# Performance work log

Hardware: AMD Instinct MI355X
Metric: run time of the kernel (lower is better)

The kernel has to match this reference:

```python
import jax, jax.numpy as jnp
import numpy as np
from jax import lax

D_MODEL = 1024
D_INNER = 2 * D_MODEL          # expand=2
D_STATE = 16
D_CONV = 4
DT_RANK = (D_MODEL + 15) // 16  # ceil(d_model/16) = 64
B, L = 4, 2048
EPS = 1e-6


def setup_inputs() -> dict:
    key = jax.random.key(0)
    ks = jax.random.split(key, 16)
    g = lambda k, shape, s=0.02: jax.random.normal(k, shape, jnp.float32) * s
    A_init = jnp.broadcast_to(jnp.arange(1, D_STATE + 1, dtype=jnp.float32), (D_INNER, D_STATE))
    return {
        "x": jax.random.normal(ks[0], (B, L, D_MODEL), jnp.float32),
        "rms1_w": jnp.ones((D_MODEL,), jnp.float32),
        "rms2_w": jnp.ones((D_MODEL,), jnp.float32),
        "in_proj_w": g(ks[1], (2 * D_INNER, D_MODEL)),
        "conv_w": g(ks[2], (D_INNER, D_CONV), 0.1),
        "conv_b": jnp.zeros((D_INNER,), jnp.float32),
        "x_proj_w": g(ks[3], (DT_RANK + 2 * D_STATE, D_INNER)),
        "dt_proj_w": g(ks[4], (D_INNER, DT_RANK), 0.1),
        "dt_proj_b": jnp.full((D_INNER,), -4.0, jnp.float32),  # softplus -> small dt
        "A_log": jnp.log(A_init),
        "D_skip": jnp.ones((D_INNER,), jnp.float32),
        "out_proj_w": g(ks[5], (D_MODEL, D_INNER)),
        "fc1_w": g(ks[6], (2 * D_MODEL, D_MODEL)),
        "fc1_b": jnp.zeros((2 * D_MODEL,), jnp.float32),
        "fc2_w": g(ks[7], (2 * D_MODEL, 2 * D_MODEL)),
        "fc2_b": jnp.zeros((2 * D_MODEL,), jnp.float32),
        "fc3_w": g(ks[8], (D_MODEL, 2 * D_MODEL)),
        "fc3_b": jnp.zeros((D_MODEL,), jnp.float32),
    }


def _rmsnorm(h, w):
    var = jnp.mean(h.astype(jnp.float32) ** 2, axis=-1, keepdims=True)
    return (w * (h * lax.rsqrt(var + EPS))).astype(h.dtype)


def _mamba(x, in_proj_w, conv_w, conv_b, x_proj_w, dt_proj_w, dt_proj_b, A_log, D_skip, out_proj_w):
    # x: (B, L, D_MODEL)
    xz = jnp.einsum('bld,ed->ble', x, in_proj_w)            # (B, L, 2*D_INNER)
    u, z = jnp.split(xz, 2, axis=-1)                        # each (B, L, D_INNER)
    # causal depthwise conv1d over time
    u_t = jnp.transpose(u, (0, 2, 1))                       # (B, D_INNER, L)
    conv = lax.conv_general_dilated(
        u_t, conv_w[:, None, :], (1,), [(D_CONV - 1, 0)],
        dimension_numbers=('NCH', 'OIH', 'NCH'), feature_group_count=D_INNER)
    u = jax.nn.silu(jnp.transpose(conv + conv_b[None, :, None], (0, 2, 1)))  # (B, L, D_INNER)
    # input-dependent SSM params
    dbc = jnp.einsum('bld,ed->ble', u, x_proj_w)            # (B, L, DT_RANK + 2*D_STATE)
    dt, Bm, Cm = jnp.split(dbc, [DT_RANK, DT_RANK + D_STATE], axis=-1)
    dt = jax.nn.softplus(jnp.einsum('blr,dr->bld', dt, dt_proj_w) + dt_proj_b)  # (B, L, D_INNER)
    A = -jnp.exp(A_log)                                     # (D_INNER, D_STATE)

    def step(s, inp):
        d, u_i, b_i, c_i = inp                              # d,u_i:(B,Di); b_i,c_i:(B,N)
        s = s * jnp.exp(d[..., None] * A) + (d * u_i)[..., None] * b_i[:, None, :]
        y = jnp.einsum('bdn,bn->bd', s, c_i)
        return s, y

    s0 = jnp.zeros((u.shape[0], D_INNER, D_STATE), u.dtype)
    inputs = (jnp.moveaxis(dt, 1, 0), jnp.moveaxis(u, 1, 0),
              jnp.moveaxis(Bm, 1, 0), jnp.moveaxis(Cm, 1, 0))
    _, ys = lax.scan(step, s0, inputs)                      # (L, B, D_INNER)
    y = jnp.moveaxis(ys, 0, 1) + u * D_skip                 # (B, L, D_INNER)
    y = y * jax.nn.silu(z)
    return jnp.einsum('ble,de->bld', y, out_proj_w)         # (B, L, D_MODEL)


def _mlp(x, fc1_w, fc1_b, fc2_w, fc2_b, fc3_w, fc3_b):
    h = jax.nn.relu(jnp.einsum('bld,hd->blh', x, fc1_w) + fc1_b)
    h = jax.nn.relu(jnp.einsum('blh,gh->blg', h, fc2_w) + fc2_b)
    return jnp.einsum('blg,dg->bld', h, fc3_w) + fc3_b


def reference(x, rms1_w, rms2_w, in_proj_w, conv_w, conv_b, x_proj_w, dt_proj_w,
              dt_proj_b, A_log, D_skip, out_proj_w, fc1_w, fc1_b, fc2_w, fc2_b,
              fc3_w, fc3_b):
    x0 = _rmsnorm(x, rms1_w)
    x1 = _mamba(x0, in_proj_w, conv_w, conv_b, x_proj_w, dt_proj_w, dt_proj_b,
                A_log, D_skip, out_proj_w)
    x = x1 + x
    x2 = _rmsnorm(x, rms2_w)
    x3 = _mlp(x2, fc1_w, fc1_b, fc2_w, fc2_b, fc3_w, fc3_b)
    return x + x3
```

## Files before the change

### kernel.cpp

```cpp
#include <hip/hip_runtime.h>
#include <hip/hip_bf16.h>
#include <math.h>

#define D_MODEL 1024
#define D_INNER 2048
#define NSTATE 16
#define DT_RANK 64
#define NB 4
#define SEQ 2048
#define XPROJ_N 96
#define EPSV 1e-6f
#define CH 32
#define CL (SEQ/CH)

typedef __attribute__((ext_vector_type(8))) short bf16x8;
typedef __attribute__((ext_vector_type(4))) float f32x4;

__device__ __forceinline__ float sigmoidf_fast(float x) {
    return 1.f / (1.f + __expf(-x));
}

__device__ __forceinline__ ushort f2bf(float f) {
    union { float f; unsigned int u; } c; c.f = f;
    return (ushort)((c.u + 0x7FFFu + ((c.u >> 16) & 1u)) >> 16);
}

__device__ __forceinline__ float bf2f(ushort u) {
    union { unsigned int i; float f; } c; c.i = ((unsigned int)u) << 16; return c.f;
}

__device__ __forceinline__ float softplus_fast(float v) {
    return fmaxf(v, 0.f) + __logf(1.f + __expf(-fabsf(v)));
}

__device__ __forceinline__ void gload16(const ushort* g, ushort* l) {
    __builtin_amdgcn_global_load_lds(
        (const __attribute__((address_space(1))) unsigned int*)g,
        (__attribute__((address_space(3))) unsigned int*)l, 16, 0, 0);
}

__global__ __launch_bounds__(256)
void cvt_all_kernel(const float* __restrict__ s0, const float* __restrict__ s1,
                    const float* __restrict__ s2, const float* __restrict__ s3,
                    const float* __restrict__ s4, const float* __restrict__ s5,
                    ushort* __restrict__ dst) {
    const size_t i = ((size_t)blockIdx.x * 256 + threadIdx.x) * 4;
    const size_t c0 = 4194304, c1 = 6291456, c2 = 8388608,
                 c3 = 12582912, c4 = 14680064;
    const float* src;
    size_t off;
    if      (i < c0) { src = s0; off = i; }
    else if (i < c1) { src = s1; off = i - c0; }
    else if (i < c2) { src = s2; off = i - c1; }
    else if (i < c3) { src = s3; off = i - c2; }
    else if (i < c4) { src = s4; off = i - c3; }
    else             { src = s5; off = i - c4; }
    const float4 v = *(const float4*)(src + off);
    ushort4 o;
    o.x = f2bf(v.x); o.y = f2bf(v.y); o.z = f2bf(v.z); o.w = f2bf(v.w);
    *(ushort4*)(dst + i) = o;
}

__global__ __launch_bounds__(256)
void cvt_pad_xproj(const float* __restrict__ src, ushort* __restrict__ dst) {
    const int e = (blockIdx.x * 256 + threadIdx.x) * 4;
    const int row = e >> 11;
    ushort4 o = {0, 0, 0, 0};
    if (row < XPROJ_N) {
        const float4 v = *(const float4*)(src + e);
        o.x = f2bf(v.x); o.y = f2bf(v.y); o.z = f2bf(v.z); o.w = f2bf(v.w);
    }
    *(ushort4*)(dst + e) = o;
}

__global__ __launch_bounds__(256)
void rmsnorm_bf_kernel(const float* __restrict__ in,
                       const float* __restrict__ w,
                       ushort* __restrict__ out) {
    const int row = blockIdx.x;
    const float4 v = ((const float4*)(in + (size_t)row * D_MODEL))[threadIdx.x];
    float ss = v.x*v.x + v.y*v.y + v.z*v.z + v.w*v.w;
    #pragma unroll
    for (int o = 32; o > 0; o >>= 1) ss += __shfl_down(ss, o);
    __shared__ float sred[4];
    if ((threadIdx.x & 63) == 0) sred[threadIdx.x >> 6] = ss;
    __syncthreads();
    const float tot = sred[0] + sred[1] + sred[2] + sred[3];
    const float sc = rsqrtf(tot * (1.f / D_MODEL) + EPSV);
    const float4 wv = ((const float4*)w)[threadIdx.x];
    ushort4 o4;
    o4.x = f2bf(wv.x*v.x*sc); o4.y = f2bf(wv.y*v.y*sc);
    o4.z = f2bf(wv.z*v.z*sc); o4.w = f2bf(wv.w*v.w*sc);
    ((ushort4*)(out + (size_t)row * D_MODEL))[threadIdx.x] = o4;
}

#define G256_PHASE(mh, kk, STAGE, DOVM)                                           \
  {                                                                               \
    const ushort* ak = aS + (size_t)(buf * 2 + (kk)) * 8192;                      \
    const ushort* bk = bS + (size_t)(buf * 2 + (kk)) * BSLOT;                     \
    bf16x8 av0, av1, av2, av3; bf16x8 bv[NREP];                                   \
    av0 = *(const bf16x8*)&ak[(wr * 128 + ((mh)*4+0)*16 + fr) * 32 + kswz];       \
    av1 = *(const bf16x8*)&ak[(wr * 128 + ((mh)*4+1)*16 + fr) * 32 + kswz];       \
    av2 = *(const bf16x8*)&ak[(wr * 128 + ((mh)*4+2)*16 + fr) * 32 + kswz];       \
    av3 = *(const bf16x8*)&ak[(wr * 128 + ((mh)*4+3)*16 + fr) * 32 + kswz];       \
    _Pragma("unroll")                                                             \
    for (int j2 = 0; j2 < NREP; ++j2)                                             \
        bv[j2] = *(const bf16x8*)&bk[(wcol + j2*16 + fr) * 32 + kswz];            \
    STAGE                                                                         \
    __builtin_amdgcn_s_barrier();                                                 \
    asm volatile("s_waitcnt lgkmcnt(0)" ::: "memory");                            \
    __builtin_amdgcn_sched_barrier(0);                                            \
    __builtin_amdgcn_s_setprio(1);                                                \
    _Pragma("unroll")                                                             \
    for (int j2 = 0; j2 < NREP; ++j2) {                                           \
        acc[(mh)*4+0][j2] = __builtin_amdgcn_mfma_f32_16x16x32_bf16(av0, bv[j2], acc[(mh)*4+0][j2], 0,0,0); \
        acc[(mh)*4+1][j2] = __builtin_amdgcn_mfma_f32_16x16x32_bf16(av1, bv[j2], acc[(mh)*4+1][j2], 0,0,0); \
        acc[(mh)*4+2][j2] = __builtin_amdgcn_mfma_f32_16x16x32_bf16(av2, bv[j2], acc[(mh)*4+2][j2], 0,0,0); \
        acc[(mh)*4+3][j2] = __builtin_amdgcn_mfma_f32_16x16x32_bf16(av3, bv[j2], acc[(mh)*4+3][j2], 0,0,0); \
    }                                                                             \
    __builtin_amdgcn_s_setprio(0);                                                \
    if (DOVM) {                                                                   \
        if constexpr (NREP == 4) { asm volatile("s_waitcnt vmcnt(4)" ::: "memory"); } \
        else                     { asm volatile("s_waitcnt vmcnt(3)" ::: "memory"); } \
    }                                                                             \
    __builtin_amdgcn_s_barrier();                                                 \
  }

template<int NREP, bool OUTBF, int ACT, bool HASB, bool HASR>
__global__ __launch_bounds__(512, 2)
void gemm256(const ushort* __restrict__ A, int lda,
             const ushort* __restrict__ W, int ldw,
             const float* __restrict__ bias, const float* __restrict__ res,
             void* __restrict__ Cout, int N, int K, int gridN) {
    constexpr int BN = NREP * 64;
    constexpr int BSLOT = BN * 32;
    extern __shared__ ushort lds[];
    ushort* const aS = lds;
    ushort* const bS = lds + 32768;

    const int tid = threadIdx.x;
    const int w = tid >> 6, l = tid & 63;
    const int wr = w >> 2, wc = w & 3;
    const int fr = l & 15;
    const int kswz = ((l >> 4) * 8) ^ ((fr & 3) << 3);
    const int wcol = wc * (NREP * 16);

    const int nwg = (int)gridDim.x;
    const int cpx = nwg >> 3;
    const int bid = (int)blockIdx.x;
    const int swz = (bid & 7) * cpx + (bid >> 3);
    const size_t m0 = (size_t)(swz / gridN) * 256;
    const int n0 = (swz % gridN) * BN;

    const int NT = K >> 6;

    const int sr = w * 16 + (l >> 2);
    const int sc = ((l & 3) * 8) ^ (((l >> 2) & 3) << 3);

    auto stageA = [&](int buf2, int kk, int kt) {
        ushort* slot = aS + (size_t)(buf2 * 2 + kk) * 8192;
        const ushort* g = A + (m0 + sr) * (size_t)lda + kt * 64 + kk * 32 + sc;
        gload16(g, slot + w * 512);
        gload16(g + (size_t)128 * lda, slot + 4096 + w * 512);
    };
    auto stageB = [&](int buf2, int kk, int kt) {
        ushort* slot = bS + (size_t)(buf2 * 2 + kk) * BSLOT;
        const ushort* g = W + ((size_t)n0 + sr) * ldw + kt * 64 + kk * 32 + sc;
        gload16(g, slot + w * 512);
        if (NREP == 4) gload16(g + (size_t)128 * ldw, slot + 4096 + w * 512);
    };

    f32x4 acc[8][NREP] = {};

    stageA(0, 0, 0); stageB(0, 0, 0);
    stageA(0, 1, 0); stageB(0, 1, 0);
    stageA(1, 0, 1); stageB(1, 0, 1);
    if constexpr (NREP == 4) { asm volatile("s_waitcnt vmcnt(4)" ::: "memory"); }
    else                     { asm volatile("s_waitcnt vmcnt(3)" ::: "memory"); }
    __builtin_amdgcn_s_barrier();

    int buf = 0;
    for (int t = 0; t < NT; ++t, buf ^= 1) {
        const bool s1 = (t + 1 < NT), s2 = (t + 2 < NT);
        G256_PHASE(0, 0, { if (s1) stageA(buf ^ 1, 1, t + 1); }, false)
        G256_PHASE(0, 1, { if (s1) stageB(buf ^ 1, 1, t + 1); }, false)
        G256_PHASE(1, 0, { }, false)
        G256_PHASE(1, 1, { if (s2) { stageA(buf, 0, t + 2); stageB(buf, 0, t + 2); } }, true)
    }

    const int r0 = (l >> 4) * 4;
    #pragma unroll
    for (int mi = 0; mi < 8; ++mi) {
        #pragma unroll
        for (int i = 0; i < 4; ++i) {
            const size_t grow = m0 + wr * 128 + mi * 16 + r0 + i;
            #pragma unroll
            for (int ni = 0; ni < NREP; ++ni) {
                const int gcol = n0 + wcol + ni * 16 + fr;
                float v = acc[mi][ni][i];
                if (HASB) v += bias[gcol];
                if (ACT == 1) v = fmaxf(v, 0.f);
                if (ACT == 2) v = softplus_fast(v);
                if (HASR) v += res[grow * N + gcol];
                if (OUTBF) ((ushort*)Cout)[grow * N + gcol] = f2bf(v);
                else       ((float*)Cout)[grow * N + gcol] = v;
            }
        }
    }
}

template<bool OUTBF, int ACT, bool HASB, bool HASR>
__global__ __launch_bounds__(256)
void gemm_mfma(const ushort* __restrict__ A, int lda,
               const ushort* __restrict__ W, int ldw,
               const float* __restrict__ bias, const float* __restrict__ res,
               void* __restrict__ Cout, int N, int K) {
    __shared__ ushort sA[128 * 32];
    __shared__ ushort sB[128 * 32];
    const int tid = threadIdx.x;
    const int w = tid >> 6, l = tid & 63;
    const size_t m0 = (size_t)blockIdx.y * 128;
    const int n0 = blockIdx.x * 128;
    const int wm = (w >> 1) * 64, wn = (w & 1) * 64;
    f32x4 acc[4][4] = {};

    const ushort* gA = A + (m0 + (size_t)(w*16 + (l >> 2))) * lda + (l & 3) * 8;
    const ushort* gB = W + ((size_t)(n0 + w*16 + (l >> 2))) * ldw + (l & 3) * 8;
    ushort* lA = &sA[w * 512];
    ushort* lB = &sB[w * 512];

    const int fr = l & 15;
    const int fk = (l >> 4) * 8;
    const int aoff0 = (wm + fr) * 32 + fk;
    const int boff0 = (wn + fr) * 32 + fk;

    for (int k0 = 0; k0 < K; k0 += 32) {
        __syncthreads();
        gload16(gA + k0, lA);
        gload16(gA + (size_t)64 * lda + k0, lA + 2048);
        gload16(gB + k0, lB);
        gload16(gB + (size_t)64 * ldw + k0, lB + 2048);
        __syncthreads();
        bf16x8 av[4], bv[4];
        #pragma unroll
        for (int i = 0; i < 4; ++i) {
            av[i] = *(const bf16x8*)&sA[aoff0 + i * 512];
            bv[i] = *(const bf16x8*)&sB[boff0 + i * 512];
        }
        #pragma unroll
        for (int mi = 0; mi < 4; ++mi)
            #pragma unroll
            for (int ni = 0; ni < 4; ++ni)
                acc[mi][ni] = __builtin_amdgcn_mfma_f32_16x16x32_bf16(
                    av[mi], bv[ni], acc[mi][ni], 0, 0, 0);
    }
    const int r0 = (l >> 4) * 4;
    #pragma unroll
    for (int mi = 0; mi < 4; ++mi) {
        #pragma unroll
        for (int i = 0; i < 4; ++i) {
            const size_t grow = m0 + wm + mi * 16 + r0 + i;
            #pragma unroll
            for (int ni = 0; ni < 4; ++ni) {
                const int gcol = n0 + wn + ni * 16 + fr;
                float v = acc[mi][ni][i];
                if (HASB) v += bias[gcol];
                if (ACT == 1) v = fmaxf(v, 0.f);
                if (ACT == 2) v = softplus_fast(v);
                if (HASR) v += res[grow * N + gcol];
                if (OUTBF) ((ushort*)Cout)[grow * N + gcol] = f2bf(v);
                else       ((float*)Cout)[grow * N + gcol] = v;
            }
        }
    }
}

__global__ __launch_bounds__(256)
void xproj_mfma(const ushort* __restrict__ A, const ushort* __restrict__ Wp,
                float* __restrict__ part) {
    __shared__ ushort sA[128 * 32];
    __shared__ ushort sB[128 * 32];
    const int tid = threadIdx.x;
    const int w = tid >> 6, l = tid & 63;
    const int kz = blockIdx.x;
    const size_t M = (size_t)gridDim.y * 128;
    const size_t m0 = (size_t)blockIdx.y * 128;
    const int wm = (w >> 1) * 64, wn = (w & 1) * 64;
    f32x4 acc[4][4] = {};

    const ushort* gA = A + (m0 + (size_t)(w*16 + (l >> 2))) * D_INNER + (l & 3) * 8;
    const ushort* gB = Wp + ((size_t)(w*16 + (l >> 2))) * D_INNER + (l & 3) * 8;
    ushort* lA = &sA[w * 512];
    ushort* lB = &sB[w * 512];

    const int fr = l & 15;
    const int fk = (l >> 4) * 8;
    const int aoff0 = (wm + fr) * 32 + fk;
    const int boff0 = (wn + fr) * 32 + fk;

    const int kbeg = kz * 512, kend = kbeg + 512;
    for (int k0 = kbeg; k0 < kend; k0 += 32) {
        __syncthreads();
        gload16(gA + k0, lA);
        gload16(gA + (size_t)64 * D_INNER + k0, lA + 2048);
        gload16(gB + k0, lB);
        gload16(gB + (size_t)64 * D_INNER + k0, lB + 2048);
        __syncthreads();
        bf16x8 av[4], bv[4];
        #pragma unroll
        for (int i = 0; i < 4; ++i) {
            av[i] = *(const bf16x8*)&sA[aoff0 + i * 512];
            bv[i] = *(const bf16x8*)&sB[boff0 + i * 512];
        }
        #pragma unroll
        for (int mi = 0; mi < 4; ++mi)
            #pragma unroll
            for (int ni = 0; ni < 4; ++ni)
                acc[mi][ni] = __builtin_amdgcn_mfma_f32_16x16x32_bf16(
                    av[mi], bv[ni], acc[mi][ni], 0, 0, 0);
    }
    float* my = part + (size_t)kz * M * XPROJ_N;
    const int r0 = (l >> 4) * 4;
    #pragma unroll
    for (int mi = 0; mi < 4; ++mi) {
        #pragma unroll
        for (int i = 0; i < 4; ++i) {
            const size_t grow = m0 + wm + mi * 16 + r0 + i;
            #pragma unroll
            for (int ni = 0; ni < 4; ++ni) {
                const int gcol = wn + ni * 16 + fr;
                if (gcol < XPROJ_N)
                    my[grow * XPROJ_N + gcol] = acc[mi][ni][i];
            }
        }
    }
}

__global__ __launch_bounds__(256)
void xproj_reduce(const float* __restrict__ part, ushort* __restrict__ dbc, int M) {
    const size_t q = (size_t)blockIdx.x * 256 + threadIdx.x;
    const size_t nq = (size_t)M * XPROJ_N / 4;
    if (q >= nq) return;
    const float4* p = (const float4*)part;
    float4 s = p[q];
    const float4 s1 = p[q + nq];
    const float4 s2 = p[q + 2*nq];
    const float4 s3 = p[q + 3*nq];
    s.x += s1.x + s2.x + s3.x;
    s.y += s1.y + s2.y + s3.y;
    s.z += s1.z + s2.z + s3.z;
    s.w += s1.w + s2.w + s3.w;
    ushort4 o;
    o.x = f2bf(s.x); o.y = f2bf(s.y); o.z = f2bf(s.z); o.w = f2bf(s.w);
    ((ushort4*)dbc)[q] = o;
}

__global__ __launch_bounds__(256)
void conv_silu_kernel(const ushort* __restrict__ u_raw, int ldu,
                      const float* __restrict__ cw,
                      const float* __restrict__ cb,
                      ushort* __restrict__ out) {
    const int idx = (blockIdx.x * 256 + threadIdx.x) * 4;
    const int d = idx & (D_INNER - 1);
    const int row = idx >> 11;
    const int l = row & (SEQ - 1);
    const ushort* up = u_raw + (size_t)row * ldu + d;
    const float4 cb4 = *(const float4*)(cb + d);
    float acc[4];
    float4 wq[4];
    #pragma unroll
    for (int j = 0; j < 4; ++j) wq[j] = *(const float4*)(cw + (d + j) * 4);
    ushort4 t = *(const ushort4*)up;
    acc[0] = fmaf(wq[0].w, bf2f(t.x), cb4.x);
    acc[1] = fmaf(wq[1].w, bf2f(t.y), cb4.y);
    acc[2] = fmaf(wq[2].w, bf2f(t.z), cb4.z);
    acc[3] = fmaf(wq[3].w, bf2f(t.w), cb4.w);
    if (l >= 1) {
        t = *(const ushort4*)(up - ldu);
        acc[0] = fmaf(wq[0].z, bf2f(t.x), acc[0]);
        acc[1] = fmaf(wq[1].z, bf2f(t.y), acc[1]);
        acc[2] = fmaf(wq[2].z, bf2f(t.z), acc[2]);
        acc[3] = fmaf(wq[3].z, bf2f(t.w), acc[3]);
    }
    if (l >= 2) {
        t = *(const ushort4*)(up - 2 * ldu);
        acc[0] = fmaf(wq[0].y, bf2f(t.x), acc[0]);
        acc[1] = fmaf(wq[1].y, bf2f(t.y), acc[1]);
        acc[2] = fmaf(wq[2].y, bf2f(t.z), acc[2]);
        acc[3] = fmaf(wq[3].y, bf2f(t.w), acc[3]);
    }
    if (l >= 3) {
        t = *(const ushort4*)(up - 3 * ldu);
        acc[0] = fmaf(wq[0].x, bf2f(t.x), acc[0]);
        acc[1] = fmaf(wq[1].x, bf2f(t.y), acc[1]);
        acc[2] = fmaf(wq[2].x, bf2f(t.z), acc[2]);
        acc[3] = fmaf(wq[3].x, bf2f(t.w), acc[3]);
    }
    ushort4 o;
    o.x = f2bf(acc[0] * sigmoidf_fast(acc[0]));
    o.y = f2bf(acc[1] * sigmoidf_fast(acc[1]));
    o.z = f2bf(acc[2] * sigmoidf_fast(acc[2]));
    o.w = f2bf(acc[3] * sigmoidf_fast(acc[3]));
    *(ushort4*)(out + (size_t)row * D_INNER + d) = o;
}

__global__ __launch_bounds__(256)
void scan_pass1(const ushort* __restrict__ dt, const ushort* __restrict__ u,
                const ushort* __restrict__ dbc, const float* __restrict__ A_log,
                float* __restrict__ cP, float* __restrict__ cR) {
    const int bid = blockIdx.x;
    const int dblk = bid & 7;
    const int c = (bid >> 3) & (CH - 1);
    const int b = bid >> 8;
    const int d = dblk * 256 + threadIdx.x;
    float Av[NSTATE];
    #pragma unroll
    for (int q = 0; q < 4; ++q) {
        const float4 al = *(const float4*)(A_log + d * NSTATE + q * 4);
        Av[q*4+0] = -__expf(al.x);
        Av[q*4+1] = -__expf(al.y);
        Av[q*4+2] = -__expf(al.z);
        Av[q*4+3] = -__expf(al.w);
    }
    float P[NSTATE], R[NSTATE];
    #pragma unroll
    for (int n = 0; n < NSTATE; ++n) { P[n] = 1.f; R[n] = 0.f; }
    const int l0 = c * CL;
    for (int i = 0; i < CL; ++i) {
        const size_t trow = (size_t)b * SEQ + l0 + i;
        const float dtv = bf2f(dt[trow * D_INNER + d]);
        const float uv  = bf2f(u[trow * D_INNER + d]);
        const float dtu = dtv * uv;
        const ushort* Brow = dbc + trow * XPROJ_N + DT_RANK;
        #pragma unroll
        for (int n = 0; n < NSTATE; ++n) {
            const float a = __expf(dtv * Av[n]);
            P[n] *= a;
            R[n] = fmaf(R[n], a, dtu * bf2f(Brow[n]));
        }
    }
    const size_t base = (((size_t)b * CH + c) * NSTATE) * D_INNER + d;
    #pragma unroll
    for (int n = 0; n < NSTATE; ++n) {
        cP[base + (size_t)n * D_INNER] = P[n];
        cR[base + (size_t)n * D_INNER] = R[n];
    }
}

__global__ __launch_bounds__(256)
void scan_combine(const float* __restrict__ cP, const float* __restrict__ cR,
                  float* __restrict__ cS) {
    const int idx = blockIdx.x * 256 + threadIdx.x;
    const int d = idx & (D_INNER - 1);
    const int n = (idx >> 11) & (NSTATE - 1);
    const int b = idx >> 15;
    float s = 0.f;
    for (int c = 0; c < CH; ++c) {
        const size_t off = (((size_t)b * CH + c) * NSTATE + n) * D_INNER + d;
        cS[off] = s;
        s = fmaf(cP[off], s, cR[off]);
    }
}

__global__ __launch_bounds__(256)
void scan_pass2(const ushort* __restrict__ dt, const ushort* __restrict__ u,
                const ushort* __restrict__ dbc, const float* __restrict__ A_log,
                const float* __restrict__ Dskip, const ushort* __restrict__ z, int ldz,
                const float* __restrict__ cS, ushort* __restrict__ yout) {
    const int bid = blockIdx.x;
    const int dblk = bid & 7;
    const int c = (bid >> 3) & (CH - 1);
    const int b = bid >> 8;
    const int d = dblk * 256 + threadIdx.x;
    float Av[NSTATE];
    #pragma unroll
    for (int q = 0; q < 4; ++q) {
        const float4 al = *(const float4*)(A_log + d * NSTATE + q * 4);
        Av[q*4+0] = -__expf(al.x);
        Av[q*4+1] = -__expf(al.y);
        Av[q*4+2] = -__expf(al.z);
        Av[q*4+3] = -__expf(al.w);
    }
    const float Dsk = Dskip[d];
    float s[NSTATE];
    const size_t sbase = (((size_t)b * CH + c) * NSTATE) * D_INNER + d;
    #pragma unroll
    for (int n = 0; n < NSTATE; ++n) s[n] = cS[sbase + (size_t)n * D_INNER];
    const int l0 = c * CL;
    for (int i = 0; i < CL; ++i) {
        const size_t trow = (size_t)b * SEQ + l0 + i;
        const float dtv = bf2f(dt[trow * D_INNER + d]);
        const float uv  = bf2f(u[trow * D_INNER + d]);
        const float dtu = dtv * uv;
        const ushort* Brow = dbc + trow * XPROJ_N + DT_RANK;
        const ushort* Crow = Brow + NSTATE;
        float y = 0.f;
        #pragma unroll
        for (int n = 0; n < NSTATE; ++n) {
            const float a = __expf(dtv * Av[n]);
            s[n] = fmaf(s[n], a, dtu * bf2f(Brow[n]));
            y = fmaf(s[n], bf2f(Crow[n]), y);
        }
        const float zv = bf2f(z[trow * ldz + d]);
        const float yf = (y + uv * Dsk) * (zv * sigmoidf_fast(zv));
        yout[trow * D_INNER + d] = f2bf(yf);
    }
}

extern "C" void kernel_launch(void* const* d_in, const int* in_sizes, int n_in,
                              void* d_out, int out_size, void* d_ws, size_t ws_size,
                              hipStream_t stream) {
    const float* x         = (const float*)d_in[0];
    const float* rms1_w    = (const float*)d_in[1];
    const float* rms2_w    = (const float*)d_in[2];
    const float* in_proj_w = (const float*)d_in[3];
    const float* conv_w    = (const float*)d_in[4];
    const float* conv_b    = (const float*)d_in[5];
    const float* x_proj_w  = (const float*)d_in[6];
    const float* dt_proj_w = (const float*)d_in[7];
    const float* dt_proj_b = (const float*)d_in[8];
    const float* A_log     = (const float*)d_in[9];
    const float* D_skip    = (const float*)d_in[10];
    const float* out_proj_w= (const float*)d_in[11];
    const float* fc1_w     = (const float*)d_in[12];
    const float* fc1_b     = (const float*)d_in[13];
    const float* fc2_w     = (const float*)d_in[14];
    const float* fc2_b     = (const float*)d_in[15];
    const float* fc3_w     = (const float*)d_in[16];
    const float* fc3_b     = (const float*)d_in[17];
    float* out = (float*)d_out;

    hipFuncSetAttribute(reinterpret_cast<const void*>(&gemm256<4,true,0,false,false>),
                        hipFuncAttributeMaxDynamicSharedMemorySize, 131072);
    hipFuncSetAttribute(reinterpret_cast<const void*>(&gemm256<4,true,1,true,false>),
                        hipFuncAttributeMaxDynamicSharedMemorySize, 131072);
    hipFuncSetAttribute(reinterpret_cast<const void*>(&gemm256<2,false,0,false,true>),
                        hipFuncAttributeMaxDynamicSharedMemorySize, 98304);
    hipFuncSetAttribute(reinterpret_cast<const void*>(&gemm256<2,false,0,true,true>),
                        hipFuncAttributeMaxDynamicSharedMemorySize, 98304);

    char* ws = (char*)d_ws;
    size_t woff = 0;
    ushort* wInProj  = (ushort*)(ws + woff); woff += (size_t)4096*1024*2;
    ushort* wOutProj = (ushort*)(ws + woff); woff += (size_t)1024*2048*2;
    ushort* wFc1     = (ushort*)(ws + woff); woff += (size_t)2048*1024*2;
    ushort* wFc2     = (ushort*)(ws + woff); woff += (size_t)2048*2048*2;
    ushort* wFc3     = (ushort*)(ws + woff); woff += (size_t)1024*2048*2;
    ushort* wDt      = (ushort*)(ws + woff); woff += (size_t)2048*64*2;
    ushort* wXp      = (ushort*)(ws + woff); woff += (size_t)128*2048*2;

    auto need = [woff](size_t BC) -> size_t {
        const size_t T = BC * SEQ;
        return woff
             + T * 4096 * 2
             + 3ull * (T * D_INNER * 2)
             + T * XPROJ_N * 2
             + 4ull * (T * XPROJ_N * 4)
             + 3ull * (BC * CH * NSTATE * D_INNER * 4);
    };
    int BC = 4;
    if (ws_size < need(4)) BC = 2;
    if (ws_size < need(2)) BC = 1;
    const size_t T = (size_t)BC * SEQ;

    const size_t szXz = T * 4096 * 2;
    const size_t szBf = T * D_INNER * 2;
    const size_t szDbc = T * XPROJ_N * 2;
    const size_t szPart = 4ull * T * XPROJ_N * 4;
    const size_t szP = (size_t)BC * CH * NSTATE * D_INNER * 4;
    ushort* xz   = (ushort*)(ws + woff);
    ushort* cbuf = (ushort*)(ws + woff + szXz);
    ushort* ubuf = (ushort*)(ws + woff + szXz + szBf);
    ushort* xbf  = (ushort*)(ws + woff + szXz + 2*szBf);
    ushort* dbc  = (ushort*)(ws + woff + szXz + 3*szBf);
    float*  part = (float*)(ws + woff + szXz + 3*szBf + szDbc);
    float*  cP   = (float*)(ws + woff + szXz + 3*szBf + szDbc + szPart);
    float*  cR   = (float*)(ws + woff + szXz + 3*szBf + szDbc + szPart + szP);
    float*  cS   = (float*)(ws + woff + szXz + 3*szBf + szDbc + szPart + 2*szP);
    ushort* h1bf = xz;
    ushort* h2bf = cbuf;

    const dim3 b256(256);
    const int scanGrid = BC * CH * (D_INNER / 256);
    const int combGrid = BC * NSTATE * D_INNER / 256;
    const int gM = (int)(T / 256);

    cvt_all_kernel<<<dim3(14464), b256, 0, stream>>>(
        in_proj_w, out_proj_w, fc1_w, fc2_w, fc3_w, dt_proj_w, wInProj);
    cvt_pad_xproj<<<dim3(256), b256, 0, stream>>>(x_proj_w, wXp);

    for (int cb = 0; cb < NB; cb += BC) {
        const float* xc = x + (size_t)cb * SEQ * D_MODEL;
        float* outc = out + (size_t)cb * SEQ * D_MODEL;
        rmsnorm_bf_kernel<<<(int)T, b256, 0, stream>>>(xc, rms1_w, xbf);
        gemm256<4,true,0,false,false><<<dim3(gM * 16), 512, 131072, stream>>>(
            xbf, D_MODEL, wInProj, D_MODEL, nullptr, nullptr, xz, 4096, D_MODEL, 16);
        conv_silu_kernel<<<(int)(T*D_INNER/1024), b256, 0, stream>>>(xz, 4096, conv_w, conv_b, cbuf);
        xproj_mfma<<<dim3(4, T/128), b256, 0, stream>>>(cbuf, wXp, part);
        xproj_reduce<<<dim3((unsigned)((T*XPROJ_N/4 + 255)/256)), b256, 0, stream>>>(part, dbc, (int)T);
        gemm_mfma<true,2,true,false><<<dim3(D_INNER/128, T/128), b256, 0, stream>>>(
            dbc, XPROJ_N, wDt, DT_RANK, dt_proj_b, nullptr, ubuf, D_INNER, DT_RANK);
        scan_pass1<<<scanGrid, b256, 0, stream>>>(ubuf, cbuf, dbc, A_log, cP, cR);
        scan_combine<<<combGrid, b256, 0, stream>>>(cP, cR, cS);
        scan_pass2<<<scanGrid, b256, 0, stream>>>(ubuf, cbuf, dbc, A_log, D_skip,
                                                  xz + D_INNER, 4096, cS, xbf);
        gemm256<2,false,0,false,true><<<dim3(gM * 8), 512, 98304, stream>>>(
            xbf, D_INNER, wOutProj, D_INNER, nullptr, xc, outc, D_MODEL, D_INNER, 8);
    }

    for (int cb = 0; cb < NB; cb += BC) {
        float* outc = out + (size_t)cb * SEQ * D_MODEL;
        rmsnorm_bf_kernel<<<(int)T, b256, 0, stream>>>(outc, rms2_w, xbf);
        gemm256<4,true,1,true,false><<<dim3(gM * 8), 512, 131072, stream>>>(
            xbf, D_MODEL, wFc1, D_MODEL, fc1_b, nullptr, h1bf, 2*D_MODEL, D_MODEL, 8);
        gemm256<4,true,1,true,false><<<dim3(gM * 8), 512, 131072, stream>>>(
            h1bf, 2*D_MODEL, wFc2, 2*D_MODEL, fc2_b, nullptr, h2bf, 2*D_MODEL, 2*D_MODEL, 8);
        gemm256<2,false,0,true,true><<<dim3(gM * 8), 512, 98304, stream>>>(
            h2bf, 2*D_MODEL, wFc3, 2*D_MODEL, fc3_b, outc, outc, D_MODEL, 2*D_MODEL, 8);
    }
}
```

Baseline: 757.8 us.

## Split scan state dimension across two half-waves and vectorize B/C loads

The chunked selective-scan passes now give each channel to two lanes, each handling 8 of the 16 states, so twice as many threads cover the work. In pass 2 the partial y values are combined with a cross-half shuffle. The per-step B and C row reads become single 16-byte vector loads. The aim is more parallelism and fewer serial exp/FMA per thread, at the cost of duplicated dt/u/z loads across the two halves and half the lanes sitting idle during the output write.

```diff
diff --git a/kernel.cpp b/kernel.cpp
--- a/kernel.cpp
+++ b/kernel.cpp
@@ -14,6 +14,7 @@
 #define CL (SEQ/CH)
 
 typedef __attribute__((ext_vector_type(8))) short bf16x8;
+typedef __attribute__((ext_vector_type(8))) unsigned short u16x8;
 typedef __attribute__((ext_vector_type(4))) float f32x4;
 
 __device__ __forceinline__ float sigmoidf_fast(float x) {
@@ -409,39 +410,41 @@
                 const ushort* __restrict__ dbc, const float* __restrict__ A_log,
                 float* __restrict__ cP, float* __restrict__ cR) {
     const int bid = blockIdx.x;
-    const int dblk = bid & 7;
-    const int c = (bid >> 3) & (CH - 1);
-    const int b = bid >> 8;
-    const int d = dblk * 256 + threadIdx.x;
-    float Av[NSTATE];
-    #pragma unroll
-    for (int q = 0; q < 4; ++q) {
-        const float4 al = *(const float4*)(A_log + d * NSTATE + q * 4);
-        Av[q*4+0] = -__expf(al.x);
-        Av[q*4+1] = -__expf(al.y);
-        Av[q*4+2] = -__expf(al.z);
-        Av[q*4+3] = -__expf(al.w);
-    }
-    float P[NSTATE], R[NSTATE];
-    #pragma unroll
-    for (int n = 0; n < NSTATE; ++n) { P[n] = 1.f; R[n] = 0.f; }
+    const int dblk = bid & 15;
+    const int c = (bid >> 4) & (CH - 1);
+    const int b = bid >> 9;
+    const int wv = threadIdx.x >> 6, l = threadIdx.x & 63;
+    const int dl = l & 31, half = l >> 5;
+    const int d = dblk * 128 + wv * 32 + dl;
+    const int nbase = half * 8;
+
+    float Av[8];
+    {
+        const float4 a0 = *(const float4*)(A_log + d * NSTATE + nbase);
+        const float4 a1 = *(const float4*)(A_log + d * NSTATE + nbase + 4);
+        Av[0] = -__expf(a0.x); Av[1] = -__expf(a0.y); Av[2] = -__expf(a0.z); Av[3] = -__expf(a0.w);
+        Av[4] = -__expf(a1.x); Av[5] = -__expf(a1.y); Av[6] = -__expf(a1.z); Av[7] = -__expf(a1.w);
+    }
+    float P[8], R[8];
+    #pragma unroll
+    for (int n = 0; n < 8; ++n) { P[n] = 1.f; R[n] = 0.f; }
     const int l0 = c * CL;
     for (int i = 0; i < CL; ++i) {
         const size_t trow = (size_t)b * SEQ + l0 + i;
         const float dtv = bf2f(dt[trow * D_INNER + d]);
         const float uv  = bf2f(u[trow * D_INNER + d]);
         const float dtu = dtv * uv;
-        const ushort* Brow = dbc + trow * XPROJ_N + DT_RANK;
-        #pragma unroll
-        for (int n = 0; n < NSTATE; ++n) {
+        const u16x8 Bv = *(const u16x8*)(dbc + trow * XPROJ_N + DT_RANK + nbase);
+        #pragma unroll
+        for (int n = 0; n < 8; ++n) {
             const float a = __expf(dtv * Av[n]);
             P[n] *= a;
-            R[n] = fmaf(R[n], a, dtu * bf2f(Brow[n]));
-        }
-    }
-    const size_t base = (((size_t)b * CH + c) * NSTATE) * D_INNER + d;
-    #pragma unroll
-    for (int n = 0; n < NSTATE; ++n) {
+            R[n] = fmaf(R[n], a, dtu * bf2f(Bv[n]));
+        }
+    }
+    const size_t base = (((size_t)b * CH + c) * NSTATE + nbase) * D_INNER + d;
+    #pragma unroll
+    for (int n = 0; n < 8; ++n) {
         cP[base + (size_t)n * D_INNER] = P[n];
         cR[base + (size_t)n * D_INNER] = R[n];
     }
@@ -468,42 +471,47 @@
                 const float* __restrict__ Dskip, const ushort* __restrict__ z, int ldz,
                 const float* __restrict__ cS, ushort* __restrict__ yout) {
     const int bid = blockIdx.x;
-    const int dblk = bid & 7;
-    const int c = (bid >> 3) & (CH - 1);
-    const int b = bid >> 8;
-    const int d = dblk * 256 + threadIdx.x;
-    float Av[NSTATE];
-    #pragma unroll
-    for (int q = 0; q < 4; ++q) {
-        const float4 al = *(const float4*)(A_log + d * NSTATE + q * 4);
-        Av[q*4+0] = -__expf(al.x);
-        Av[q*4+1] = -__expf(al.y);
-        Av[q*4+2] = -__expf(al.z);
-        Av[q*4+3] = -__expf(al.w);
+    const int dblk = bid & 15;
+    const int c = (bid >> 4) & (CH - 1);
+    const int b = bid >> 9;
+    const int wv = threadIdx.x >> 6, l = threadIdx.x & 63;
+    const int dl = l & 31, half = l >> 5;
+    const int d = dblk * 128 + wv * 32 + dl;
+    const int nbase = half * 8;
+
+    float Av[8];
+    {
+        const float4 a0 = *(const float4*)(A_log + d * NSTATE + nbase);
+        const float4 a1 = *(const float4*)(A_log + d * NSTATE + nbase + 4);
+        Av[0] = -__expf(a0.x); Av[1] = -__expf(a0.y); Av[2] = -__expf(a0.z); Av[3] = -__expf(a0.w);
+        Av[4] = -__expf(a1.x); Av[5] = -__expf(a1.y); Av[6] = -__expf(a1.z); Av[7] = -__expf(a1.w);
     }
     const float Dsk = Dskip[d];
-    float s[NSTATE];
-    const size_t sbase = (((size_t)b * CH + c) * NSTATE) * D_INNER + d;
-    #pragma unroll
-    for (int n = 0; n < NSTATE; ++n) s[n] = cS[sbase + (size_t)n * D_INNER];
+    float s[8];
+    const size_t sbase = (((size_t)b * CH + c) * NSTATE + nbase) * D_INNER + d;
+    #pragma unroll
+    for (int n = 0; n < 8; ++n) s[n] = cS[sbase + (size_t)n * D_INNER];
     const int l0 = c * CL;
     for (int i = 0; i < CL; ++i) {
         const size_t trow = (size_t)b * SEQ + l0 + i;
         const float dtv = bf2f(dt[trow * D_INNER + d]);
         const float uv  = bf2f(u[trow * D_INNER + d]);
         const float dtu = dtv * uv;
-        const ushort* Brow = dbc + trow * XPROJ_N + DT_RANK;
-        const ushort* Crow = Brow + NSTATE;
+        const u16x8 Bv = *(const u16x8*)(dbc + trow * XPROJ_N + DT_RANK + nbase);
+        const u16x8 Cv = *(const u16x8*)(dbc + trow * XPROJ_N + DT_RANK + NSTATE + nbase);
         float y = 0.f;
         #pragma unroll
-        for (int n = 0; n < NSTATE; ++n) {
+        for (int n = 0; n < 8; ++n) {
             const float a = __expf(dtv * Av[n]);
-            s[n] = fmaf(s[n], a, dtu * bf2f(Brow[n]));
-            y = fmaf(s[n], bf2f(Crow[n]), y);
-        }
-        const float zv = bf2f(z[trow * ldz + d]);
-        const float yf = (y + uv * Dsk) * (zv * sigmoidf_fast(zv));
-        yout[trow * D_INNER + d] = f2bf(yf);
+            s[n] = fmaf(s[n], a, dtu * bf2f(Bv[n]));
+            y = fmaf(s[n], bf2f(Cv[n]), y);
+        }
+        y += __shfl_xor(y, 32, 64);
+        if (half == 0) {
+            const float zv = bf2f(z[trow * ldz + d]);
+            const float yf = (y + uv * Dsk) * (zv * sigmoidf_fast(zv));
+            yout[trow * D_INNER + d] = f2bf(yf);
+        }
     }
 }
 
@@ -581,7 +589,7 @@
     ushort* h2bf = cbuf;
 
     const dim3 b256(256);
-    const int scanGrid = BC * CH * (D_INNER / 256);
+    const int scanGrid = BC * CH * 16;
     const int combGrid = BC * NSTATE * D_INNER / 256;
     const int gM = (int)(T / 256);
 
```

Measured after the change: 748.1 us. Within noise of the previous version (-1.3%).
